# Kernel tuning notes

Hardware: AMD Instinct MI355X
Metric: run time of the kernel (lower is better)

Reference implementation:

```python
import jax, jax.numpy as jnp
import numpy as np

NEG = -1e9  # stand-in for -inf in masked_fill; avoids NaN rows for never-gathered states


def _residual(x, w1, b1, w2, b2):
    # ResidualLayerOld: two relu linears with a residual connection (eval mode, no dropout)
    h = jax.nn.relu(x @ w1.T + b1)
    return x + jax.nn.relu(h @ w2.T + b2)


def setup_inputs() -> dict:
    key = jax.random.key(0)
    B, T, V, C, H, SPW = 16, 256, 32000, 1024, 512, 8
    ks = jax.random.split(key, 32)
    s = 0.05  # keep logits in a sane range
    inp = {
        'start_emb': jax.random.normal(ks[0], (C, H), jnp.float32) * s,
        'start_l1w': jax.random.normal(ks[1], (H, H), jnp.float32) * s,
        'start_l1b': jnp.zeros((H,), jnp.float32),
        'start_l2w': jax.random.normal(ks[2], (H, H), jnp.float32) * s,
        'start_l2b': jnp.zeros((H,), jnp.float32),
        'start_ow': jax.random.normal(ks[3], (1, H), jnp.float32) * s,
        'start_ob': jnp.zeros((1,), jnp.float32),
        'state_emb': jax.random.normal(ks[4], (C, H), jnp.float32) * s,
        'trans_l1w': jax.random.normal(ks[5], (H, H), jnp.float32) * s,
        'trans_l1b': jnp.zeros((H,), jnp.float32),
        'trans_l2w': jax.random.normal(ks[6], (H, H), jnp.float32) * s,
        'trans_l2b': jnp.zeros((H,), jnp.float32),
        'proj_w': jax.random.normal(ks[7], (C, H), jnp.float32) * s,
        'pret_emb': jax.random.normal(ks[8], (C, H), jnp.float32) * s,
        'term_l1w': jax.random.normal(ks[9], (H, H), jnp.float32) * s,
        'term_l1b': jnp.zeros((H,), jnp.float32),
        'term_l2w': jax.random.normal(ks[10], (H, H), jnp.float32) * s,
        'term_l2b': jnp.zeros((H,), jnp.float32),
        'term_ow': jax.random.normal(ks[11], (V, H), jnp.float32) * s,
        'term_ob': jnp.zeros((V,), jnp.float32),
        'text': jax.random.randint(ks[12], (B, T), 0, V, jnp.int32),
        'word2state': jax.random.randint(ks[13], (V, SPW), 0, C, jnp.int32),
    }
    return inp


def reference(start_emb, start_l1w, start_l1b, start_l2w, start_l2b, start_ow, start_ob,
              state_emb, trans_l1w, trans_l1b, trans_l2w, trans_l2b, proj_w,
              pret_emb, term_l1w, term_l1b, term_l2w, term_l2b, term_ow, term_ob,
              text, word2state):
    C, H = start_emb.shape
    V, SPW = word2state.shape

    # start: MLP(C,H)->(C,1) -> log_softmax over C
    start = jax.nn.log_softmax(
        (_residual(start_emb, start_l1w, start_l1b, start_l2w, start_l2b) @ start_ow.T + start_ob).squeeze(-1))

    # transition: [C,C] log_softmax over next state
    trans = jax.nn.log_softmax(
        _residual(state_emb, trans_l1w, trans_l1b, trans_l2w, trans_l2b) @ proj_w.T, axis=-1)

    # emission: [C,V] logits, masked to the sparse word->state assignment, log_softmax over V
    term_logits = _residual(pret_emb, term_l1w, term_l1b, term_l2w, term_l2b) @ term_ow.T + term_ob
    mask = jnp.zeros((C, V), bool).at[word2state.reshape(-1), jnp.repeat(jnp.arange(V), SPW)].set(True)
    emission = jax.nn.log_softmax(jnp.where(mask, term_logits, NEG), axis=-1)

    # clamp: gather per-timestep [SPW,SPW] transition blocks + emissions
    cs = word2state[text]                               # [B,T,SPW]
    pot = trans[cs[:, :-1, :, None], cs[:, 1:, None, :]]  # [B,T-1,SPW,SPW] (prev i, next j)
    init = start[cs[:, 0]]                              # [B,SPW]
    obs = emission[cs, text[:, :, None]]                # [B,T,SPW]
    pot = pot.at[:, 0].add((init + obs[:, 0])[:, :, None])
    pot = pot + obs[:, 1:][:, :, None, :]               # add obs_{t+1} along next-state j
    pot = jnp.swapaxes(pot, -1, -2)                     # [B,T-1,next,prev], as in clamp()

    # forward algorithm (fb kernel's alpha pass): alpha_{t+1}[n] = LSE_p pot[t,n,p] + alpha_t[p]
    def step(alpha, p):
        a = jax.nn.logsumexp(p + alpha[:, None, :], axis=-1)
        return a, None

    B = text.shape[0]
    alpha0 = jnp.zeros((B, SPW), pot.dtype)
    alphaT, _ = jax.lax.scan(step, alpha0, jnp.swapaxes(pot, 0, 1))
    evidence = jax.nn.logsumexp(alphaT, axis=-1).sum()  # full-length sequences
    return evidence
```

## Files before the change

### kernel.cpp

```cpp
#include <hip/hip_runtime.h>
#include <hip/hip_bf16.h>

#define C_DIM 1024
#define H_DIM 512
#define V_DIM 32000
#define B_DIM 16
#define T_DIM 256
#define SPW   8
#define NSLOT 32

typedef unsigned short u16;
typedef unsigned int   u32;
typedef __attribute__((ext_vector_type(8))) short bf16x8;
typedef __attribute__((ext_vector_type(4))) float f32x4;

__device__ __forceinline__ u16 f2b(float f) {
    union { float f; u32 i; } x; x.f = f;
    u32 i = x.i;
    i += 0x7fffu + ((i >> 16) & 1u);
    return (u16)(i >> 16);
}
__device__ __forceinline__ float b2f(u16 u) {
    union { u32 i; float f; } x; x.i = ((u32)u) << 16; return x.f;
}
__device__ __forceinline__ float dot8_bf16(uint4 u, const float4 tw0, const float4 tw1) {
    return tw0.x * b2f((u16)(u.x & 0xffff)) + tw0.y * b2f((u16)(u.x >> 16))
         + tw0.z * b2f((u16)(u.y & 0xffff)) + tw0.w * b2f((u16)(u.y >> 16))
         + tw1.x * b2f((u16)(u.z & 0xffff)) + tw1.y * b2f((u16)(u.z >> 16))
         + tw1.z * b2f((u16)(u.w & 0xffff)) + tw1.w * b2f((u16)(u.w >> 16));
}

struct CvtArgs {
    const float* src[10];
    u16*         dst[10];
    int          n[10];
    float*       zero;
    int          zn;
};

__global__ __launch_bounds__(256) void cvt_kern(CvtArgs a)
{
    int seg = blockIdx.y;
    if (seg == 10) {
        for (int i = blockIdx.x * 256 + threadIdx.x; i < a.zn; i += gridDim.x * 256)
            a.zero[i] = 0.0f;
        return;
    }
    const float4* s = (const float4*)a.src[seg];
    ushort4* d = (ushort4*)a.dst[seg];
    int n4 = a.n[seg] >> 2;
    for (int i = blockIdx.x * 256 + threadIdx.x; i < n4; i += gridDim.x * 256) {
        float4 v = s[i];
        ushort4 o;
        o.x = f2b(v.x); o.y = f2b(v.y); o.z = f2b(v.z); o.w = f2b(v.w);
        d[i] = o;
    }
}

struct Mlp16Args {
    const u16*   A[3];
    const u16*   W[3];
    const float* bias[3];
    const u16*   resid[3];
    u16*         out[3];
};

__global__ __launch_bounds__(256) void mlp16_kern(Mlp16Args args)
{
    const int N = H_DIM, K = H_DIM;
    int z = blockIdx.z;
    const u16* A = args.A[z];
    const u16* B = args.W[z];
    const float* bias = args.bias[z];
    const u16* resid = args.resid[z];
    u16* out = args.out[z];

    __shared__ __align__(16) u16 As[64][40];
    __shared__ __align__(16) u16 Bs[64][40];
    int tid  = threadIdx.x;
    int m0 = blockIdx.x * 64, n0 = blockIdx.y * 64;
    int wave = tid >> 6, lane = tid & 63;
    int wr = wave >> 1, wc = wave & 1;
    int srow = tid >> 2, scol = (tid & 3) << 3;
    int quad = lane >> 4, l16 = lane & 15;
    f32x4 acc[2][2] = {};

    for (int k0 = 0; k0 < K; k0 += 32) {
        uint4 av = *(const uint4*)(A + (size_t)(m0 + srow) * K + k0 + scol);
        uint4 bv = *(const uint4*)(B + (size_t)(n0 + srow) * K + k0 + scol);
        __syncthreads();
        *(uint4*)&As[srow][scol] = av;
        *(uint4*)&Bs[srow][scol] = bv;
        __syncthreads();
        bf16x8 af0 = *(const bf16x8*)&As[wr * 32 + l16][quad * 8];
        bf16x8 af1 = *(const bf16x8*)&As[wr * 32 + 16 + l16][quad * 8];
        bf16x8 bf0 = *(const bf16x8*)&Bs[wc * 32 + l16][quad * 8];
        bf16x8 bf1 = *(const bf16x8*)&Bs[wc * 32 + 16 + l16][quad * 8];
        acc[0][0] = __builtin_amdgcn_mfma_f32_16x16x32_bf16(af0, bf0, acc[0][0], 0, 0, 0);
        acc[0][1] = __builtin_amdgcn_mfma_f32_16x16x32_bf16(af0, bf1, acc[0][1], 0, 0, 0);
        acc[1][0] = __builtin_amdgcn_mfma_f32_16x16x32_bf16(af1, bf0, acc[1][0], 0, 0, 0);
        acc[1][1] = __builtin_amdgcn_mfma_f32_16x16x32_bf16(af1, bf1, acc[1][1], 0, 0, 0);
    }
#pragma unroll
    for (int sm = 0; sm < 2; sm++)
#pragma unroll
        for (int sn = 0; sn < 2; sn++) {
            int n = n0 + wc * 32 + sn * 16 + l16;
            float bv = bias[n];
#pragma unroll
            for (int reg = 0; reg < 4; reg++) {
                int m = m0 + wr * 32 + sm * 16 + quad * 4 + reg;
                float v = fmaxf(acc[sm][sn][reg] + bv, 0.0f);
                if (resid) v += b2f(resid[(size_t)m * N + n]);
                out[(size_t)m * N + n] = f2b(v);
            }
        }
}

__global__ __launch_bounds__(256) void gemm16_kern(
    const u16* __restrict__ A, const u16* __restrict__ B,
    float* __restrict__ out, int M, int N, int K)
{
    __shared__ __align__(16) u16 As[64][40];
    __shared__ __align__(16) u16 Bs[64][40];
    int tid  = threadIdx.x;
    int m0 = blockIdx.x * 64, n0 = blockIdx.y * 64;
    int wave = tid >> 6, lane = tid & 63;
    int wr = wave >> 1, wc = wave & 1;
    int srow = tid >> 2, scol = (tid & 3) << 3;
    int quad = lane >> 4, l16 = lane & 15;
    f32x4 acc[2][2] = {};

    for (int k0 = 0; k0 < K; k0 += 32) {
        uint4 av = *(const uint4*)(A + (size_t)(m0 + srow) * K + k0 + scol);
        uint4 bv = *(const uint4*)(B + (size_t)(n0 + srow) * K + k0 + scol);
        __syncthreads();
        *(uint4*)&As[srow][scol] = av;
        *(uint4*)&Bs[srow][scol] = bv;
        __syncthreads();
        bf16x8 af0 = *(const bf16x8*)&As[wr * 32 + l16][quad * 8];
        bf16x8 af1 = *(const bf16x8*)&As[wr * 32 + 16 + l16][quad * 8];
        bf16x8 bf0 = *(const bf16x8*)&Bs[wc * 32 + l16][quad * 8];
        bf16x8 bf1 = *(const bf16x8*)&Bs[wc * 32 + 16 + l16][quad * 8];
        acc[0][0] = __builtin_amdgcn_mfma_f32_16x16x32_bf16(af0, bf0, acc[0][0], 0, 0, 0);
        acc[0][1] = __builtin_amdgcn_mfma_f32_16x16x32_bf16(af0, bf1, acc[0][1], 0, 0, 0);
        acc[1][0] = __builtin_amdgcn_mfma_f32_16x16x32_bf16(af1, bf0, acc[1][0], 0, 0, 0);
        acc[1][1] = __builtin_amdgcn_mfma_f32_16x16x32_bf16(af1, bf1, acc[1][1], 0, 0, 0);
    }
#pragma unroll
    for (int sm = 0; sm < 2; sm++)
#pragma unroll
        for (int sn = 0; sn < 2; sn++) {
            int n = n0 + wc * 32 + sn * 16 + l16;
#pragma unroll
            for (int reg = 0; reg < 4; reg++) {
                int m = m0 + wr * 32 + sm * 16 + quad * 4 + reg;
                out[(size_t)m * N + n] = acc[sm][sn][reg];
            }
        }
}

__global__ __launch_bounds__(256) void startlog_kern(
    const u16* __restrict__ Rstart16, const float* __restrict__ sow,
    const float* __restrict__ sob, float* __restrict__ startv,
    float* __restrict__ Ssum)
{
    int wid = threadIdx.x >> 6, lane = threadIdx.x & 63;
    int c = blockIdx.x * 4 + wid;
    uint4 rv = ((const uint4*)(Rstart16 + (size_t)c * H_DIM))[lane];
    const float4* wp = (const float4*)(sow);
    float4 w0 = wp[lane * 2], w1 = wp[lane * 2 + 1];
    float d = dot8_bf16(rv, w0, w1);
    for (int off = 1; off < 64; off <<= 1) d += __shfl_xor(d, off, 64);
    if (lane == 0) {
        d += sob[0];
        startv[c] = d;
        atomicAdd(Ssum + (blockIdx.x & (NSLOT - 1)), expf(d));
    }
}

__global__ __launch_bounds__(256) void rowlse_kern(const float* __restrict__ TL,
                                                   float* __restrict__ rowlse)
{
    int wid = threadIdx.x >> 6, lane = threadIdx.x & 63;
    int row = blockIdx.x * 4 + wid;
    const float4* p = (const float4*)(TL + (size_t)row * C_DIM);
    float s = 0.0f;
#pragma unroll
    for (int k = 0; k < 4; k++) {
        float4 v = p[lane + 64 * k];
        s += expf(v.x) + expf(v.y) + expf(v.z) + expf(v.w);
    }
    for (int off = 1; off < 64; off <<= 1) s += __shfl_xor(s, off, 64);
    if (lane == 0) rowlse[row] = logf(s);
}

__global__ __launch_bounds__(256) void zsum_kern(
    const u16* __restrict__ Rterm16, const float* __restrict__ tow,
    const float* __restrict__ tob, const int* __restrict__ w2s,
    float* __restrict__ Zpart)
{
    int wid = threadIdx.x >> 6, lane = threadIdx.x & 63;
    int v = blockIdx.x * 4 + wid;
    float* slot = Zpart + (blockIdx.x & (NSLOT - 1)) * C_DIM;
    const float4* twp = (const float4*)(tow + (size_t)v * H_DIM);
    float4 tw0 = twp[lane * 2], tw1 = twp[lane * 2 + 1];
    float ob = tob[v];
    int cs[SPW];
#pragma unroll
    for (int s = 0; s < SPW; s++) cs[s] = w2s[v * SPW + s];
    uint4 rv[SPW];
#pragma unroll
    for (int s = 0; s < SPW; s++)
        rv[s] = ((const uint4*)(Rterm16 + (size_t)cs[s] * H_DIM))[lane];
    float d[SPW];
#pragma unroll
    for (int s = 0; s < SPW; s++) {
        d[s] = dot8_bf16(rv[s], tw0, tw1);
        d[s] += __shfl_xor(d[s], 1, 64);
        d[s] += __shfl_xor(d[s], 2, 64);
        d[s] += __shfl_xor(d[s], 4, 64);
    }
    float x = d[0];
    int myc = cs[0];
#pragma unroll
    for (int s = 1; s < SPW; s++) {
        if ((lane & 7) == s) { x = d[s]; myc = cs[s]; }
    }
    x += __shfl_xor(x, 8, 64);
    x += __shfl_xor(x, 16, 64);
    x += __shfl_xor(x, 32, 64);
    u32 dupmask = 0;
#pragma unroll
    for (int s = 1; s < SPW; s++) {
        bool dp = false;
#pragma unroll
        for (int s2 = 0; s2 < s; s2++) dp = dp || (cs[s2] == cs[s]);
        if (dp) dupmask |= (1u << s);
    }
    if (lane < 8 && !((dupmask >> lane) & 1u))
        atomicAdd(slot + myc, expf(x + ob));
}

__global__ __launch_bounds__(256) void obs_kern(
    const u16* __restrict__ Rterm16, const float* __restrict__ tow,
    const float* __restrict__ tob, const int* __restrict__ w2s,
    const int* __restrict__ text, const float* __restrict__ Zpart,
    float* __restrict__ obs)
{
    int wid = threadIdx.x >> 6, lane = threadIdx.x & 63;
    int idx = blockIdx.x * 4 + wid;
    int v = text[idx];
    const float4* twp = (const float4*)(tow + (size_t)v * H_DIM);
    float4 tw0 = twp[lane * 2], tw1 = twp[lane * 2 + 1];
    float ob = tob[v];
    int cs[SPW];
#pragma unroll
    for (int s = 0; s < SPW; s++) cs[s] = w2s[v * SPW + s];
    uint4 rv[SPW];
#pragma unroll
    for (int s = 0; s < SPW; s++)
        rv[s] = ((const uint4*)(Rterm16 + (size_t)cs[s] * H_DIM))[lane];
    float d[SPW];
#pragma unroll
    for (int s = 0; s < SPW; s++) {
        d[s] = dot8_bf16(rv[s], tw0, tw1);
        d[s] += __shfl_xor(d[s], 1, 64);
        d[s] += __shfl_xor(d[s], 2, 64);
        d[s] += __shfl_xor(d[s], 4, 64);
    }
    float x = d[0];
    int myc = cs[0];
#pragma unroll
    for (int s = 1; s < SPW; s++) {
        if ((lane & 7) == s) { x = d[s]; myc = cs[s]; }
    }
    x += __shfl_xor(x, 8, 64);
    x += __shfl_xor(x, 16, 64);
    x += __shfl_xor(x, 32, 64);
    int g = lane >> 3;
    float zp = 0.0f;
#pragma unroll
    for (int k = 0; k < 4; k++)
        zp += Zpart[(size_t)(g * 4 + k) * C_DIM + myc];
    zp += __shfl_xor(zp, 8, 64);
    zp += __shfl_xor(zp, 16, 64);
    zp += __shfl_xor(zp, 32, 64);
    if (lane < 8)
        obs[idx * SPW + lane] = x + ob - logf(zp);
}

__device__ __forceinline__ float lsm_combine(float accv, float mv, int i, int j)
{
    float x[8];
#pragma unroll
    for (int k = 0; k < 8; k++) {
        float a = __shfl(accv, k * 8 + i, 64);
        float b = __shfl(mv,  j * 8 + k, 64);
        x[k] = a + b;
    }
    float mx = fmaxf(fmaxf(fmaxf(x[0], x[1]), fmaxf(x[2], x[3])),
                     fmaxf(fmaxf(x[4], x[5]), fmaxf(x[6], x[7])));
    float s = 0.0f;
#pragma unroll
    for (int k = 0; k < 8; k++) s += expf(x[k] - mx);
    return mx + logf(s);
}

__global__ __launch_bounds__(256) void scanA_kern(
    const float* __restrict__ TL, const float* __restrict__ rowlse,
    const float* __restrict__ obs, const float* __restrict__ startv,
    const float* __restrict__ Ssum, const int* __restrict__ text,
    const int* __restrict__ w2s, float* __restrict__ Mc)
{
    int wid = threadIdx.x >> 6, lane = threadIdx.x & 63;
    int g = blockIdx.x * 4 + wid;
    int b = g >> 4, c = g & 15;
    int t0 = c * 16;
    int cnt = min(16, (T_DIM - 1) - t0);
    int i = lane & 7, j = lane >> 3;

    const int* txt = text + b * T_DIM;
    const float* obsb = obs + (size_t)b * T_DIM * SPW;

    float logS = 0.0f;
    if (t0 == 0) {
        float ss = 0.0f;
#pragma unroll
        for (int k = 0; k < NSLOT; k++) ss += Ssum[k];
        logS = logf(ss);
    }

    auto potval = [&](int t) -> float {
        int vt  = txt[t];
        int vt1 = txt[t + 1];
        int ci = w2s[vt * SPW + i];
        int cj = w2s[vt1 * SPW + j];
        float p = TL[(size_t)ci * C_DIM + cj] - rowlse[ci] + obsb[(t + 1) * SPW + j];
        if (t == 0) p += startv[ci] - logS + obsb[i];
        return p;
    };

    float acc = potval(t0);
    if (cnt > 1) {
        float nv = potval(t0 + 1);
        for (int t = t0 + 1; t < t0 + cnt; t++) {
            float nv2 = (t + 1 < t0 + cnt) ? potval(t + 1) : 0.0f;
            acc = lsm_combine(acc, nv, i, j);
            nv = nv2;
        }
    }
    Mc[(size_t)g * 64 + lane] = acc;
}

__global__ __launch_bounds__(1024) void scanB_kern(const float* __restrict__ Mc,
                                                   float* __restrict__ out)
{
    int wave = threadIdx.x >> 6, lane = threadIdx.x & 63;
    int i = lane & 7, j = lane >> 3;
    const float* base = Mc + (size_t)wave * 16 * 64;
    float acc = base[lane];
    for (int c = 1; c < 16; c++)
        acc = lsm_combine(acc, base[(size_t)c * 64 + lane], i, j);
    float mx = acc;
    for (int o = 1; o < 64; o <<= 1) mx = fmaxf(mx, __shfl_xor(mx, o, 64));
    float e = expf(acc - mx);
    for (int o = 1; o < 64; o <<= 1) e += __shfl_xor(e, o, 64);
    __shared__ float part[16];
    if (lane == 0) part[wave] = mx + logf(e);
    __syncthreads();
    if (threadIdx.x == 0) {
        float s = 0.0f;
#pragma unroll
        for (int k = 0; k < 16; k++) s += part[k];
        out[0] = s;
    }
}

extern "C" void kernel_launch(void* const* d_in, const int* in_sizes, int n_in,
                              void* d_out, int out_size, void* d_ws, size_t ws_size,
                              hipStream_t stream)
{
    const float* start_emb = (const float*)d_in[0];
    const float* start_l1w = (const float*)d_in[1];
    const float* start_l1b = (const float*)d_in[2];
    const float* start_l2w = (const float*)d_in[3];
    const float* start_l2b = (const float*)d_in[4];
    const float* start_ow  = (const float*)d_in[5];
    const float* start_ob  = (const float*)d_in[6];
    const float* state_emb = (const float*)d_in[7];
    const float* trans_l1w = (const float*)d_in[8];
    const float* trans_l1b = (const float*)d_in[9];
    const float* trans_l2w = (const float*)d_in[10];
    const float* trans_l2b = (const float*)d_in[11];
    const float* proj_w    = (const float*)d_in[12];
    const float* pret_emb  = (const float*)d_in[13];
    const float* term_l1w  = (const float*)d_in[14];
    const float* term_l1b  = (const float*)d_in[15];
    const float* term_l2w  = (const float*)d_in[16];
    const float* term_l2b  = (const float*)d_in[17];
    const float* term_ow   = (const float*)d_in[18];
    const float* term_ob   = (const float*)d_in[19];
    const int*   text      = (const int*)d_in[20];
    const int*   w2s       = (const int*)d_in[21];

    char* w = (char*)d_ws;
    const u32 MB = 1u << 20;
    const size_t CH = (size_t)C_DIM * H_DIM;
    const size_t HH = (size_t)H_DIM * H_DIM;

    u16* emb16   = (u16*)(w);
    u16* w16     = (u16*)(w + 3u * MB);
    u16* proj16  = (u16*)(w + 6u * MB);
    u16* H16     = (u16*)(w + 7u * MB);
    u16* R16     = (u16*)(w + 10u * MB);
    float* TL    = (float*)(w + 13u * MB);
    float* startv  = (float*)(w + 17u * MB);
    float* rowlse  = (float*)(w + 17u * MB + 4096);
    float* obs     = (float*)(w + 17u * MB + 8192);
    float* Mc      = (float*)(w + 17u * MB + 8192 + 131072);
    float* Zpart   = (float*)(w + 18u * MB);
    float* Ssum    = Zpart + (size_t)NSLOT * C_DIM;

    u16* semb16 = emb16;
    u16* temb16 = emb16 + CH;
    u16* pemb16 = emb16 + 2 * CH;
    u16* sl1w16 = w16;
    u16* sl2w16 = w16 + HH;
    u16* tl1w16 = w16 + 2 * HH;
    u16* tl2w16 = w16 + 3 * HH;
    u16* ml1w16 = w16 + 4 * HH;
    u16* ml2w16 = w16 + 5 * HH;
    u16* Hs = H16, *Ht = H16 + CH, *Hp = H16 + 2 * CH;
    u16* Rstart16 = R16;
    u16* Rtrans16 = R16 + CH;
    u16* Rterm16  = R16 + 2 * CH;

    dim3 blk256(256);

    CvtArgs cv;
    cv.src[0] = start_emb; cv.dst[0] = semb16; cv.n[0] = (int)CH;
    cv.src[1] = state_emb; cv.dst[1] = temb16; cv.n[1] = (int)CH;
    cv.src[2] = pret_emb;  cv.dst[2] = pemb16; cv.n[2] = (int)CH;
    cv.src[3] = start_l1w; cv.dst[3] = sl1w16; cv.n[3] = (int)HH;
    cv.src[4] = start_l2w; cv.dst[4] = sl2w16; cv.n[4] = (int)HH;
    cv.src[5] = trans_l1w; cv.dst[5] = tl1w16; cv.n[5] = (int)HH;
    cv.src[6] = trans_l2w; cv.dst[6] = tl2w16; cv.n[6] = (int)HH;
    cv.src[7] = term_l1w;  cv.dst[7] = ml1w16; cv.n[7] = (int)HH;
    cv.src[8] = term_l2w;  cv.dst[8] = ml2w16; cv.n[8] = (int)HH;
    cv.src[9] = proj_w;    cv.dst[9] = proj16; cv.n[9] = (int)CH;
    cv.zero = Zpart; cv.zn = NSLOT * C_DIM + NSLOT;
    cvt_kern<<<dim3(128, 11), blk256, 0, stream>>>(cv);

    Mlp16Args l1 = {{semb16, temb16, pemb16},
                    {sl1w16, tl1w16, ml1w16},
                    {start_l1b, trans_l1b, term_l1b},
                    {nullptr, nullptr, nullptr},
                    {Hs, Ht, Hp}};
    Mlp16Args l2 = {{Hs, Ht, Hp},
                    {sl2w16, tl2w16, ml2w16},
                    {start_l2b, trans_l2b, term_l2b},
                    {semb16, temb16, pemb16},
                    {Rstart16, Rtrans16, Rterm16}};
    mlp16_kern<<<dim3(16, 8, 3), blk256, 0, stream>>>(l1);
    mlp16_kern<<<dim3(16, 8, 3), blk256, 0, stream>>>(l2);

    gemm16_kern<<<dim3(16, 16), blk256, 0, stream>>>(Rtrans16, proj16, TL,
                                                     C_DIM, C_DIM, H_DIM);

    startlog_kern<<<C_DIM / 4, blk256, 0, stream>>>(Rstart16, start_ow, start_ob,
                                                    startv, Ssum);
    zsum_kern<<<V_DIM / 4, blk256, 0, stream>>>(Rterm16, term_ow, term_ob, w2s, Zpart);
    rowlse_kern<<<C_DIM / 4, blk256, 0, stream>>>(TL, rowlse);
    obs_kern<<<B_DIM * T_DIM / 4, blk256, 0, stream>>>(Rterm16, term_ow, term_ob, w2s,
                                                       text, Zpart, obs);
    scanA_kern<<<B_DIM * 16 / 4, blk256, 0, stream>>>(TL, rowlse, obs, startv, Ssum,
                                                      text, w2s, Mc);
    scanB_kern<<<1, 1024, 0, stream>>>(Mc, (float*)d_out);
}
```

Baseline: 246.0 us.

## Fuse bf16 conversion into GEMM loads, double-buffer LDS, fold rowLSE into GEMM epilogue

Removes the standalone fp32-to-bf16 conversion kernel: the MLP and projection GEMMs now read fp32 inputs directly and convert them while staging into LDS. The GEMM main loops are double-buffered so global loads overlap MFMA work, with one barrier per step instead of two. The row log-sum-exp kernel is replaced by exp-sum atomics in the transition GEMM epilogue, and the start-logit kernel is merged into the zsum launch. The aim is fewer launches and less intermediate memory traffic. The cost is redundant conversion work across tiles, atomics on the row sums, and no max subtraction in the exp-sum.

New measurement: 265.0 us. 1.08x slower.

```diff
diff --git a/kernel.cpp b/kernel.cpp
--- a/kernel.cpp
+++ b/kernel.cpp
@@ -29,55 +29,42 @@
          + tw1.x * b2f((u16)(u.z & 0xffff)) + tw1.y * b2f((u16)(u.z >> 16))
          + tw1.z * b2f((u16)(u.w & 0xffff)) + tw1.w * b2f((u16)(u.w >> 16));
 }
-
-struct CvtArgs {
-    const float* src[10];
-    u16*         dst[10];
-    int          n[10];
+__device__ __forceinline__ uint4 cvt8(const float* p) {
+    float4 a = *(const float4*)p, b = *(const float4*)(p + 4);
+    uint4 r;
+    r.x = (u32)f2b(a.x) | ((u32)f2b(a.y) << 16);
+    r.y = (u32)f2b(a.z) | ((u32)f2b(a.w) << 16);
+    r.z = (u32)f2b(b.x) | ((u32)f2b(b.y) << 16);
+    r.w = (u32)f2b(b.z) | ((u32)f2b(b.w) << 16);
+    return r;
+}
+
+struct Mlp1Args {
+    const float* A[3];
+    const float* W[3];
+    const float* bias[3];
+    u16*         out[3];
     float*       zero;
     int          zn;
 };
 
-__global__ __launch_bounds__(256) void cvt_kern(CvtArgs a)
-{
-    int seg = blockIdx.y;
-    if (seg == 10) {
-        for (int i = blockIdx.x * 256 + threadIdx.x; i < a.zn; i += gridDim.x * 256)
-            a.zero[i] = 0.0f;
+__global__ __launch_bounds__(256) void mlp1_kern(Mlp1Args args)
+{
+    if (blockIdx.z == 3) {
+        int idx = (blockIdx.y * 16 + blockIdx.x) * 256 + threadIdx.x;
+        for (int i = idx; i < args.zn; i += 128 * 256) args.zero[i] = 0.0f;
         return;
     }
-    const float4* s = (const float4*)a.src[seg];
-    ushort4* d = (ushort4*)a.dst[seg];
-    int n4 = a.n[seg] >> 2;
-    for (int i = blockIdx.x * 256 + threadIdx.x; i < n4; i += gridDim.x * 256) {
-        float4 v = s[i];
-        ushort4 o;
-        o.x = f2b(v.x); o.y = f2b(v.y); o.z = f2b(v.z); o.w = f2b(v.w);
-        d[i] = o;
-    }
-}
-
-struct Mlp16Args {
-    const u16*   A[3];
-    const u16*   W[3];
-    const float* bias[3];
-    const u16*   resid[3];
-    u16*         out[3];
-};
-
-__global__ __launch_bounds__(256) void mlp16_kern(Mlp16Args args)
-{
-    const int N = H_DIM, K = H_DIM;
+    const int K = H_DIM;
     int z = blockIdx.z;
-    const u16* A = args.A[z];
-    const u16* B = args.W[z];
+    const float* A = args.A[z];
+    const float* W = args.W[z];
     const float* bias = args.bias[z];
-    const u16* resid = args.resid[z];
     u16* out = args.out[z];
 
-    __shared__ __align__(16) u16 As[64][40];
-    __shared__ __align__(16) u16 Bs[64][40];
-    int tid  = threadIdx.x;
+    __shared__ __align__(16) u16 As[2][64][40];
+    __shared__ __align__(16) u16 Bs[2][64][40];
+    int tid = threadIdx.x;
     int m0 = blockIdx.x * 64, n0 = blockIdx.y * 64;
     int wave = tid >> 6, lane = tid & 63;
     int wr = wave >> 1, wc = wave & 1;
@@ -85,21 +72,39 @@
     int quad = lane >> 4, l16 = lane & 15;
     f32x4 acc[2][2] = {};
 
-    for (int k0 = 0; k0 < K; k0 += 32) {
-        uint4 av = *(const uint4*)(A + (size_t)(m0 + srow) * K + k0 + scol);
-        uint4 bv = *(const uint4*)(B + (size_t)(n0 + srow) * K + k0 + scol);
-        __syncthreads();
-        *(uint4*)&As[srow][scol] = av;
-        *(uint4*)&Bs[srow][scol] = bv;
-        __syncthreads();
-        bf16x8 af0 = *(const bf16x8*)&As[wr * 32 + l16][quad * 8];
-        bf16x8 af1 = *(const bf16x8*)&As[wr * 32 + 16 + l16][quad * 8];
-        bf16x8 bf0 = *(const bf16x8*)&Bs[wc * 32 + l16][quad * 8];
-        bf16x8 bf1 = *(const bf16x8*)&Bs[wc * 32 + 16 + l16][quad * 8];
+    const float* ap = A + (size_t)(m0 + srow) * K + scol;
+    const float* bp = W + (size_t)(n0 + srow) * K + scol;
+
+    *(uint4*)&As[0][srow][scol] = cvt8(ap);
+    *(uint4*)&Bs[0][srow][scol] = cvt8(bp);
+    __syncthreads();
+    int cur = 0;
+#pragma unroll 1
+    for (int k0 = 0; k0 + 32 < K; k0 += 32) {
+        uint4 an = cvt8(ap + k0 + 32);
+        uint4 bn = cvt8(bp + k0 + 32);
+        bf16x8 af0 = *(const bf16x8*)&As[cur][wr * 32 + l16][quad * 8];
+        bf16x8 af1 = *(const bf16x8*)&As[cur][wr * 32 + 16 + l16][quad * 8];
+        bf16x8 bf0 = *(const bf16x8*)&Bs[cur][wc * 32 + l16][quad * 8];
+        bf16x8 bf1 = *(const bf16x8*)&Bs[cur][wc * 32 + 16 + l16][quad * 8];
         acc[0][0] = __builtin_amdgcn_mfma_f32_16x16x32_bf16(af0, bf0, acc[0][0], 0, 0, 0);
         acc[0][1] = __builtin_amdgcn_mfma_f32_16x16x32_bf16(af0, bf1, acc[0][1], 0, 0, 0);
         acc[1][0] = __builtin_amdgcn_mfma_f32_16x16x32_bf16(af1, bf0, acc[1][0], 0, 0, 0);
         acc[1][1] = __builtin_amdgcn_mfma_f32_16x16x32_bf16(af1, bf1, acc[1][1], 0, 0, 0);
+        *(uint4*)&As[cur ^ 1][srow][scol] = an;
+        *(uint4*)&Bs[cur ^ 1][srow][scol] = bn;
+        __syncthreads();
+        cur ^= 1;
+    }
+    {
+        bf16x8 af0 = *(const bf16x8*)&As[cur][wr * 32 + l16][quad * 8];
+        bf16x8 af1 = *(const bf16x8*)&As[cur][wr * 32 + 16 + l16][quad * 8];
+        bf16x8 bf0 = *(const bf16x8*)&Bs[cur][wc * 32 + l16][quad * 8];
+        bf16x8 bf1 = *(const bf16x8*)&Bs[cur][wc * 32 + 16 + l16][quad * 8];
+        acc[0][0] = __builtin_amdgcn_mfma_f32_16x16x32_bf16(af0, bf0, acc[0][0], 0, 0, 0);
+        acc[0][1] = __builtin_amdgcn_mfma_f32_16x16x32_bf16(af0, bf1, acc[0][1], 0, 0, 0);
+        acc[1][0] = __builtin_amdgcn_mfma_f32_16x16x32_bf16(af1, bf0, acc[1][0], 0, 0, 0);
+        acc[1][1] = __builtin_amdgcn_mfma_f32_16x16x32_bf16(af1, bf1, acc[1][1], 0, 0, 0);
     }
 #pragma unroll
     for (int sm = 0; sm < 2; sm++)
@@ -110,20 +115,32 @@
 #pragma unroll
             for (int reg = 0; reg < 4; reg++) {
                 int m = m0 + wr * 32 + sm * 16 + quad * 4 + reg;
-                float v = fmaxf(acc[sm][sn][reg] + bv, 0.0f);
-                if (resid) v += b2f(resid[(size_t)m * N + n]);
-                out[(size_t)m * N + n] = f2b(v);
+                out[(size_t)m * H_DIM + n] = f2b(fmaxf(acc[sm][sn][reg] + bv, 0.0f));
             }
         }
 }
 
-__global__ __launch_bounds__(256) void gemm16_kern(
-    const u16* __restrict__ A, const u16* __restrict__ B,
-    float* __restrict__ out, int M, int N, int K)
-{
-    __shared__ __align__(16) u16 As[64][40];
-    __shared__ __align__(16) u16 Bs[64][40];
-    int tid  = threadIdx.x;
+struct Mlp2Args {
+    const u16*   A[3];
+    const float* W[3];
+    const float* bias[3];
+    const float* resid[3];
+    u16*         out[3];
+};
+
+__global__ __launch_bounds__(256) void mlp2_kern(Mlp2Args args)
+{
+    const int K = H_DIM;
+    int z = blockIdx.z;
+    const u16* A = args.A[z];
+    const float* W = args.W[z];
+    const float* bias = args.bias[z];
+    const float* resid = args.resid[z];
+    u16* out = args.out[z];
+
+    __shared__ __align__(16) u16 As[2][64][40];
+    __shared__ __align__(16) u16 Bs[2][64][40];
+    int tid = threadIdx.x;
     int m0 = blockIdx.x * 64, n0 = blockIdx.y * 64;
     int wave = tid >> 6, lane = tid & 63;
     int wr = wave >> 1, wc = wave & 1;
@@ -131,76 +148,149 @@
     int quad = lane >> 4, l16 = lane & 15;
     f32x4 acc[2][2] = {};
 
-    for (int k0 = 0; k0 < K; k0 += 32) {
-        uint4 av = *(const uint4*)(A + (size_t)(m0 + srow) * K + k0 + scol);
-        uint4 bv = *(const uint4*)(B + (size_t)(n0 + srow) * K + k0 + scol);
-        __syncthreads();
-        *(uint4*)&As[srow][scol] = av;
-        *(uint4*)&Bs[srow][scol] = bv;
-        __syncthreads();
-        bf16x8 af0 = *(const bf16x8*)&As[wr * 32 + l16][quad * 8];
-        bf16x8 af1 = *(const bf16x8*)&As[wr * 32 + 16 + l16][quad * 8];
-        bf16x8 bf0 = *(const bf16x8*)&Bs[wc * 32 + l16][quad * 8];
-        bf16x8 bf1 = *(const bf16x8*)&Bs[wc * 32 + 16 + l16][quad * 8];
+    const u16* ap = A + (size_t)(m0 + srow) * K + scol;
+    const float* bp = W + (size_t)(n0 + srow) * K + scol;
+
+    *(uint4*)&As[0][srow][scol] = *(const uint4*)ap;
+    *(uint4*)&Bs[0][srow][scol] = cvt8(bp);
+    __syncthreads();
+    int cur = 0;
+#pragma unroll 1
+    for (int k0 = 0; k0 + 32 < K; k0 += 32) {
+        uint4 an = *(const uint4*)(ap + k0 + 32);
+        uint4 bn = cvt8(bp + k0 + 32);
+        bf16x8 af0 = *(const bf16x8*)&As[cur][wr * 32 + l16][quad * 8];
+        bf16x8 af1 = *(const bf16x8*)&As[cur][wr * 32 + 16 + l16][quad * 8];
+        bf16x8 bf0 = *(const bf16x8*)&Bs[cur][wc * 32 + l16][quad * 8];
+        bf16x8 bf1 = *(const bf16x8*)&Bs[cur][wc * 32 + 16 + l16][quad * 8];
         acc[0][0] = __builtin_amdgcn_mfma_f32_16x16x32_bf16(af0, bf0, acc[0][0], 0, 0, 0);
         acc[0][1] = __builtin_amdgcn_mfma_f32_16x16x32_bf16(af0, bf1, acc[0][1], 0, 0, 0);
         acc[1][0] = __builtin_amdgcn_mfma_f32_16x16x32_bf16(af1, bf0, acc[1][0], 0, 0, 0);
         acc[1][1] = __builtin_amdgcn_mfma_f32_16x16x32_bf16(af1, bf1, acc[1][1], 0, 0, 0);
+        *(uint4*)&As[cur ^ 1][srow][scol] = an;
+        *(uint4*)&Bs[cur ^ 1][srow][scol] = bn;
+        __syncthreads();
+        cur ^= 1;
+    }
+    {
+        bf16x8 af0 = *(const bf16x8*)&As[cur][wr * 32 + l16][quad * 8];
+        bf16x8 af1 = *(const bf16x8*)&As[cur][wr * 32 + 16 + l16][quad * 8];
+        bf16x8 bf0 = *(const bf16x8*)&Bs[cur][wc * 32 + l16][quad * 8];
+        bf16x8 bf1 = *(const bf16x8*)&Bs[cur][wc * 32 + 16 + l16][quad * 8];
+        acc[0][0] = __builtin_amdgcn_mfma_f32_16x16x32_bf16(af0, bf0, acc[0][0], 0, 0, 0);
+        acc[0][1] = __builtin_amdgcn_mfma_f32_16x16x32_bf16(af0, bf1, acc[0][1], 0, 0, 0);
+        acc[1][0] = __builtin_amdgcn_mfma_f32_16x16x32_bf16(af1, bf0, acc[1][0], 0, 0, 0);
+        acc[1][1] = __builtin_amdgcn_mfma_f32_16x16x32_bf16(af1, bf1, acc[1][1], 0, 0, 0);
     }
 #pragma unroll
     for (int sm = 0; sm < 2; sm++)
 #pragma unroll
         for (int sn = 0; sn < 2; sn++) {
             int n = n0 + wc * 32 + sn * 16 + l16;
+            float bv = bias[n];
 #pragma unroll
             for (int reg = 0; reg < 4; reg++) {
                 int m = m0 + wr * 32 + sm * 16 + quad * 4 + reg;
-                out[(size_t)m * N + n] = acc[sm][sn][reg];
+                float v = fmaxf(acc[sm][sn][reg] + bv, 0.0f) + resid[(size_t)m * H_DIM + n];
+                out[(size_t)m * H_DIM + n] = f2b(v);
             }
         }
 }
 
-__global__ __launch_bounds__(256) void startlog_kern(
+__global__ __launch_bounds__(256) void transgemm_kern(
+    const u16* __restrict__ A, const float* __restrict__ B,
+    float* __restrict__ TL, float* __restrict__ rowsum)
+{
+    const int K = H_DIM;
+    __shared__ __align__(16) u16 As[2][64][40];
+    __shared__ __align__(16) u16 Bs[2][64][40];
+    int tid = threadIdx.x;
+    int m0 = blockIdx.x * 64, n0 = blockIdx.y * 64;
+    int wave = tid >> 6, lane = tid & 63;
+    int wr = wave >> 1, wc = wave & 1;
+    int srow = tid >> 2, scol = (tid & 3) << 3;
+    int quad = lane >> 4, l16 = lane & 15;
+    f32x4 acc[2][2] = {};
+
+    const u16* ap = A + (size_t)(m0 + srow) * K + scol;
+    const float* bp = B + (size_t)(n0 + srow) * K + scol;
+
+    *(uint4*)&As[0][srow][scol] = *(const uint4*)ap;
+    *(uint4*)&Bs[0][srow][scol] = cvt8(bp);
+    __syncthreads();
+    int cur = 0;
+#pragma unroll 1
+    for (int k0 = 0; k0 + 32 < K; k0 += 32) {
+        uint4 an = *(const uint4*)(ap + k0 + 32);
+        uint4 bn = cvt8(bp + k0 + 32);
+        bf16x8 af0 = *(const bf16x8*)&As[cur][wr * 32 + l16][quad * 8];
+        bf16x8 af1 = *(const bf16x8*)&As[cur][wr * 32 + 16 + l16][quad * 8];
+        bf16x8 bf0 = *(const bf16x8*)&Bs[cur][wc * 32 + l16][quad * 8];
+        bf16x8 bf1 = *(const bf16x8*)&Bs[cur][wc * 32 + 16 + l16][quad * 8];
+        acc[0][0] = __builtin_amdgcn_mfma_f32_16x16x32_bf16(af0, bf0, acc[0][0], 0, 0, 0);
+        acc[0][1] = __builtin_amdgcn_mfma_f32_16x16x32_bf16(af0, bf1, acc[0][1], 0, 0, 0);
+        acc[1][0] = __builtin_amdgcn_mfma_f32_16x16x32_bf16(af1, bf0, acc[1][0], 0, 0, 0);
+        acc[1][1] = __builtin_amdgcn_mfma_f32_16x16x32_bf16(af1, bf1, acc[1][1], 0, 0, 0);
+        *(uint4*)&As[cur ^ 1][srow][scol] = an;
+        *(uint4*)&Bs[cur ^ 1][srow][scol] = bn;
+        __syncthreads();
+        cur ^= 1;
+    }
+    {
+        bf16x8 af0 = *(const bf16x8*)&As[cur][wr * 32 + l16][quad * 8];
+        bf16x8 af1 = *(const bf16x8*)&As[cur][wr * 32 + 16 + l16][quad * 8];
+        bf16x8 bf0 = *(const bf16x8*)&Bs[cur][wc * 32 + l16][quad * 8];
+        bf16x8 bf1 = *(const bf16x8*)&Bs[cur][wc * 32 + 16 + l16][quad * 8];
+        acc[0][0] = __builtin_amdgcn_mfma_f32_16x16x32_bf16(af0, bf0, acc[0][0], 0, 0, 0);
+        acc[0][1] = __builtin_amdgcn_mfma_f32_16x16x32_bf16(af0, bf1, acc[0][1], 0, 0, 0);
+        acc[1][0] = __builtin_amdgcn_mfma_f32_16x16x32_bf16(af1, bf0, acc[1][0], 0, 0, 0);
+        acc[1][1] = __builtin_amdgcn_mfma_f32_16x16x32_bf16(af1, bf1, acc[1][1], 0, 0, 0);
+    }
+#pragma unroll
+    for (int sm = 0; sm < 2; sm++)
+#pragma unroll
+        for (int reg = 0; reg < 4; reg++) {
+            int m = m0 + wr * 32 + sm * 16 + quad * 4 + reg;
+            float e = 0.0f;
+#pragma unroll
+            for (int sn = 0; sn < 2; sn++) {
+                int n = n0 + wc * 32 + sn * 16 + l16;
+                float v = acc[sm][sn][reg];
+                TL[(size_t)m * C_DIM + n] = v;
+                e += expf(v);
+            }
+            e += __shfl_xor(e, 1, 64);
+            e += __shfl_xor(e, 2, 64);
+            e += __shfl_xor(e, 4, 64);
+            e += __shfl_xor(e, 8, 64);
+            if (l16 == 0) atomicAdd(rowsum + m, e);
+        }
+}
+
+__global__ __launch_bounds__(256) void zsum_start_kern(
+    const u16* __restrict__ Rterm16, const float* __restrict__ tow,
+    const float* __restrict__ tob, const int* __restrict__ w2s,
+    float* __restrict__ Zpart,
     const u16* __restrict__ Rstart16, const float* __restrict__ sow,
     const float* __restrict__ sob, float* __restrict__ startv,
     float* __restrict__ Ssum)
 {
     int wid = threadIdx.x >> 6, lane = threadIdx.x & 63;
-    int c = blockIdx.x * 4 + wid;
-    uint4 rv = ((const uint4*)(Rstart16 + (size_t)c * H_DIM))[lane];
-    const float4* wp = (const float4*)(sow);
-    float4 w0 = wp[lane * 2], w1 = wp[lane * 2 + 1];
-    float d = dot8_bf16(rv, w0, w1);
-    for (int off = 1; off < 64; off <<= 1) d += __shfl_xor(d, off, 64);
-    if (lane == 0) {
-        d += sob[0];
-        startv[c] = d;
-        atomicAdd(Ssum + (blockIdx.x & (NSLOT - 1)), expf(d));
-    }
-}
-
-__global__ __launch_bounds__(256) void rowlse_kern(const float* __restrict__ TL,
-                                                   float* __restrict__ rowlse)
-{
-    int wid = threadIdx.x >> 6, lane = threadIdx.x & 63;
-    int row = blockIdx.x * 4 + wid;
-    const float4* p = (const float4*)(TL + (size_t)row * C_DIM);
-    float s = 0.0f;
-#pragma unroll
-    for (int k = 0; k < 4; k++) {
-        float4 v = p[lane + 64 * k];
-        s += expf(v.x) + expf(v.y) + expf(v.z) + expf(v.w);
-    }
-    for (int off = 1; off < 64; off <<= 1) s += __shfl_xor(s, off, 64);
-    if (lane == 0) rowlse[row] = logf(s);
-}
-
-__global__ __launch_bounds__(256) void zsum_kern(
-    const u16* __restrict__ Rterm16, const float* __restrict__ tow,
-    const float* __restrict__ tob, const int* __restrict__ w2s,
-    float* __restrict__ Zpart)
-{
-    int wid = threadIdx.x >> 6, lane = threadIdx.x & 63;
+    if (blockIdx.x >= V_DIM / 4) {
+        int bid = blockIdx.x - V_DIM / 4;
+        int c = bid * 4 + wid;
+        uint4 rv = ((const uint4*)(Rstart16 + (size_t)c * H_DIM))[lane];
+        const float4* wp = (const float4*)(sow);
+        float4 w0 = wp[lane * 2], w1 = wp[lane * 2 + 1];
+        float d = dot8_bf16(rv, w0, w1);
+        for (int off = 1; off < 64; off <<= 1) d += __shfl_xor(d, off, 64);
+        if (lane == 0) {
+            d += sob[0];
+            startv[c] = d;
+            atomicAdd(Ssum + (bid & (NSLOT - 1)), expf(d));
+        }
+        return;
+    }
     int v = blockIdx.x * 4 + wid;
     float* slot = Zpart + (blockIdx.x & (NSLOT - 1)) * C_DIM;
     const float4* twp = (const float4*)(tow + (size_t)v * H_DIM);
@@ -308,7 +398,7 @@
 }
 
 __global__ __launch_bounds__(256) void scanA_kern(
-    const float* __restrict__ TL, const float* __restrict__ rowlse,
+    const float* __restrict__ TL, const float* __restrict__ rowsum,
     const float* __restrict__ obs, const float* __restrict__ startv,
     const float* __restrict__ Ssum, const int* __restrict__ text,
     const int* __restrict__ w2s, float* __restrict__ Mc)
@@ -336,7 +426,7 @@
         int vt1 = txt[t + 1];
         int ci = w2s[vt * SPW + i];
         int cj = w2s[vt1 * SPW + j];
-        float p = TL[(size_t)ci * C_DIM + cj] - rowlse[ci] + obsb[(t + 1) * SPW + j];
+        float p = TL[(size_t)ci * C_DIM + cj] - logf(rowsum[ci]) + obsb[(t + 1) * SPW + j];
         if (t == 0) p += startv[ci] - logS + obsb[i];
         return p;
     };
@@ -407,30 +497,17 @@
     char* w = (char*)d_ws;
     const u32 MB = 1u << 20;
     const size_t CH = (size_t)C_DIM * H_DIM;
-    const size_t HH = (size_t)H_DIM * H_DIM;
-
-    u16* emb16   = (u16*)(w);
-    u16* w16     = (u16*)(w + 3u * MB);
-    u16* proj16  = (u16*)(w + 6u * MB);
-    u16* H16     = (u16*)(w + 7u * MB);
-    u16* R16     = (u16*)(w + 10u * MB);
-    float* TL    = (float*)(w + 13u * MB);
-    float* startv  = (float*)(w + 17u * MB);
-    float* rowlse  = (float*)(w + 17u * MB + 4096);
-    float* obs     = (float*)(w + 17u * MB + 8192);
-    float* Mc      = (float*)(w + 17u * MB + 8192 + 131072);
-    float* Zpart   = (float*)(w + 18u * MB);
-    float* Ssum    = Zpart + (size_t)NSLOT * C_DIM;
-
-    u16* semb16 = emb16;
-    u16* temb16 = emb16 + CH;
-    u16* pemb16 = emb16 + 2 * CH;
-    u16* sl1w16 = w16;
-    u16* sl2w16 = w16 + HH;
-    u16* tl1w16 = w16 + 2 * HH;
-    u16* tl2w16 = w16 + 3 * HH;
-    u16* ml1w16 = w16 + 4 * HH;
-    u16* ml2w16 = w16 + 5 * HH;
+
+    u16*   H16    = (u16*)(w);
+    u16*   R16    = (u16*)(w + 3u * MB);
+    float* TL     = (float*)(w + 6u * MB);
+    float* startv = (float*)(w + 10u * MB);
+    float* obs    = (float*)(w + 10u * MB + 4096);
+    float* Mc     = (float*)(w + 10u * MB + 4096 + 131072);
+    float* Zpart  = (float*)(w + 11u * MB);
+    float* Ssum   = Zpart + (size_t)NSLOT * C_DIM;
+    float* rowsum = Ssum + NSLOT;
+
     u16* Hs = H16, *Ht = H16 + CH, *Hp = H16 + 2 * CH;
     u16* Rstart16 = R16;
     u16* Rtrans16 = R16 + CH;
@@ -438,43 +515,33 @@
 
     dim3 blk256(256);
 
-    CvtArgs cv;
-    cv.src[0] = start_emb; cv.dst[0] = semb16; cv.n[0] = (int)CH;
-    cv.src[1] = state_emb; cv.dst[1] = temb16; cv.n[1] = (int)CH;
-    cv.src[2] = pret_emb;  cv.dst[2] = pemb16; cv.n[2] = (int)CH;
-    cv.src[3] = start_l1w; cv.dst[3] = sl1w16; cv.n[3] = (int)HH;
-    cv.src[4] = start_l2w; cv.dst[4] = sl2w16; cv.n[4] = (int)HH;
-    cv.src[5] = trans_l1w; cv.dst[5] = tl1w16; cv.n[5] = (int)HH;
-    cv.src[6] = trans_l2w; cv.dst[6] = tl2w16; cv.n[6] = (int)HH;
-    cv.src[7] = term_l1w;  cv.dst[7] = ml1w16; cv.n[7] = (int)HH;
-    cv.src[8] = term_l2w;  cv.dst[8] = ml2w16; cv.n[8] = (int)HH;
-    cv.src[9] = proj_w;    cv.dst[9] = proj16; cv.n[9] = (int)CH;
-    cv.zero = Zpart; cv.zn = NSLOT * C_DIM + NSLOT;
-    cvt_kern<<<dim3(128, 11), blk256, 0, stream>>>(cv);
-
-    Mlp16Args l1 = {{semb16, temb16, pemb16},
-                    {sl1w16, tl1w16, ml1w16},
-                    {start_l1b, trans_l1b, term_l1b},
-                    {nullptr, nullptr, nullptr},
-                    {Hs, Ht, Hp}};
-    Mlp16Args l2 = {{Hs, Ht, Hp},
-                    {sl2w16, tl2w16, ml2w16},
-                    {start_l2b, trans_l2b, term_l2b},
-                    {semb16, temb16, pemb16},
-                    {Rstart16, Rtrans16, Rterm16}};
-    mlp16_kern<<<dim3(16, 8, 3), blk256, 0, stream>>>(l1);
-    mlp16_kern<<<dim3(16, 8, 3), blk256, 0, stream>>>(l2);
-
-    gemm16_kern<<<dim3(16, 16), blk256, 0, stream>>>(Rtrans16, proj16, TL,
-                                                     C_DIM, C_DIM, H_DIM);
-
-    startlog_kern<<<C_DIM / 4, blk256, 0, stream>>>(Rstart16, start_ow, start_ob,
-                                                    startv, Ssum);
-    zsum_kern<<<V_DIM / 4, blk256, 0, stream>>>(Rterm16, term_ow, term_ob, w2s, Zpart);
-    rowlse_kern<<<C_DIM / 4, blk256, 0, stream>>>(TL, rowlse);
+    Mlp1Args a1;
+    a1.A[0] = start_emb; a1.A[1] = state_emb; a1.A[2] = pret_emb;
+    a1.W[0] = start_l1w; a1.W[1] = trans_l1w; a1.W[2] = term_l1w;
+    a1.bias[0] = start_l1b; a1.bias[1] = trans_l1b; a1.bias[2] = term_l1b;
+    a1.out[0] = Hs; a1.out[1] = Ht; a1.out[2] = Hp;
+    a1.zero = Zpart;
+    a1.zn = NSLOT * C_DIM + NSLOT + C_DIM;
+
+    Mlp2Args a2;
+    a2.A[0] = Hs; a2.A[1] = Ht; a2.A[2] = Hp;
+    a2.W[0] = start_l2w; a2.W[1] = trans_l2w; a2.W[2] = term_l2w;
+    a2.bias[0] = start_l2b; a2.bias[1] = trans_l2b; a2.bias[2] = term_l2b;
+    a2.resid[0] = start_emb; a2.resid[1] = state_emb; a2.resid[2] = pret_emb;
+    a2.out[0] = Rstart16; a2.out[1] = Rtrans16; a2.out[2] = Rterm16;
+
+    mlp1_kern<<<dim3(16, 8, 4), blk256, 0, stream>>>(a1);
+    mlp2_kern<<<dim3(16, 8, 3), blk256, 0, stream>>>(a2);
+
+    transgemm_kern<<<dim3(16, 16), blk256, 0, stream>>>(Rtrans16, proj_w, TL, rowsum);
+
+    zsum_start_kern<<<V_DIM / 4 + C_DIM / 4, blk256, 0, stream>>>(
+        Rterm16, term_ow, term_ob, w2s, Zpart,
+        Rstart16, start_ow, start_ob, startv, Ssum);
+
     obs_kern<<<B_DIM * T_DIM / 4, blk256, 0, stream>>>(Rterm16, term_ow, term_ob, w2s,
                                                        text, Zpart, obs);
-    scanA_kern<<<B_DIM * 16 / 4, blk256, 0, stream>>>(TL, rowlse, obs, startv, Ssum,
+    scanA_kern<<<B_DIM * 16 / 4, blk256, 0, stream>>>(TL, rowsum, obs, startv, Ssum,
                                                       text, w2s, Mc);
     scanB_kern<<<1, 1024, 0, stream>>>(Mc, (float*)d_out);
 }
```
